# Performance work log

Measured on AMD Instinct MI355X. Metric: run time of the kernel, lower is better.

## Reference

```python
import jax, jax.numpy as jnp
import numpy as np

B, C, H, W = 2, 256, 360, 360
N1 = N2 = 1024


def setup_inputs() -> dict:
    key = jax.random.key(0)
    ks = jax.random.split(key, 12)
    s = 0.02
    feature = jax.random.normal(ks[0], (B, C, H, W), dtype=jnp.float32)
    # midx rows: [batch_idx, h, w]; frame 0 centers and frame 1 centers
    idx1 = jnp.stack([
        jnp.zeros((N1,), dtype=jnp.int32),
        jax.random.randint(ks[1], (N1,), 0, H, dtype=jnp.int32),
        jax.random.randint(ks[2], (N1,), 0, W, dtype=jnp.int32),
    ])
    idx2 = jnp.stack([
        jnp.ones((N2,), dtype=jnp.int32),
        jax.random.randint(ks[3], (N2,), 0, H, dtype=jnp.int32),
        jax.random.randint(ks[4], (N2,), 0, W, dtype=jnp.int32),
    ])
    w1 = jax.random.normal(ks[5], (256, 256), dtype=jnp.float32) * s
    b1 = jnp.zeros((256,), dtype=jnp.float32)
    w2 = jax.random.normal(ks[6], (256, 128), dtype=jnp.float32) * s
    b2 = jnp.zeros((128,), dtype=jnp.float32)
    w3 = jax.random.normal(ks[7], (128, 32), dtype=jnp.float32) * s
    b3 = jnp.zeros((32,), dtype=jnp.float32)
    w4 = jax.random.normal(ks[8], (32, 1), dtype=jnp.float32) * s
    b4 = jnp.zeros((1,), dtype=jnp.float32)
    return {"feature": feature, "idx1": idx1, "idx2": idx2,
            "w1": w1, "b1": b1, "w2": w2, "b2": b2,
            "w3": w3, "b3": b3, "w4": w4, "b4": b4}


def reference(feature, idx1, idx2, w1, b1, w2, b2, w3, b3, w4, b4):
    # feature: [B,C,H,W] -> [B,H,W,C] (torch .permute(0,2,3,1))
    feat = jnp.transpose(feature, (0, 2, 3, 1))

    def project(midx):
        # irregular gather of per-center features: [N, C]
        x = feat[midx[0], midx[1], midx[2]]
        h = jax.nn.relu(x @ w1 + b1)          # [N, 256]
        return jax.nn.relu(h @ w2 + b2)       # [N, 128]

    f1 = project(idx1)                        # [N1, D]
    f2 = project(idx2)                        # [N2, D]
    # laplacian_dists: broadcast outer difference [N1, N2, D]
    diff = f1[:, None, :] - f2[None, :, :]
    # out_layer = linear_last(D, 32, 1): Linear -> ReLU -> Linear
    h = jax.nn.relu(jnp.einsum('mnd,dk->mnk', diff, w3) + b3)
    out = jnp.einsum('mnk,ko->mno', h, w4) + b4
    return out[..., 0]                        # [N1, N2] similarity
```

## Files before the change

kernel.cpp:

```cpp
#include <hip/hip_runtime.h>

#define NPTS 1024
#define NC 256
#define NH 360
#define NW 360
#define NHW (NH * NW)
#define NCHW (NC * NHW)
#define PPB 8

__global__ __launch_bounds__(256) void gather_kernel(
    const float* __restrict__ feature,
    const int* __restrict__ idx1,
    const int* __restrict__ idx2,
    float* __restrict__ X)
{
    const int point = blockIdx.x;
    const int col = point & (NPTS - 1);
    const int* idx = (point < NPTS) ? idx1 : idx2;
    const int bb = idx[col];
    const int hh = idx[NPTS + col];
    const int ww = idx[2 * NPTS + col];
    const size_t base = (size_t)bb * NCHW + (size_t)hh * NW + ww;
    const int c = threadIdx.x;
    X[(size_t)point * NC + c] = feature[base + (size_t)c * NHW];
}

__global__ __launch_bounds__(512) void mlp_kernel(
    const float* __restrict__ X,
    const float* __restrict__ w1, const float* __restrict__ b1,
    const float* __restrict__ w2, const float* __restrict__ b2,
    const float* __restrict__ w3, const float* __restrict__ b3,
    float* __restrict__ pq)
{
    __shared__ float Xs[PPB * 256];
    __shared__ float H1s[PPB * 256];
    __shared__ float F2s[PPB * 128];

    const int tid = threadIdx.x;
    const int base = blockIdx.x * PPB;

    {
        const float* src = X + (size_t)base * 256;
        #pragma unroll
        for (int i = 0; i < PPB * 256; i += 512)
            Xs[i + tid] = src[i + tid];
    }
    __syncthreads();

    {
        const int j = tid & 255;
        const int half = tid >> 8;
        float acc[4] = {0.f, 0.f, 0.f, 0.f};
        #pragma unroll 4
        for (int c = 0; c < 256; ++c) {
            float wv = w1[c * 256 + j];
            #pragma unroll
            for (int q = 0; q < 4; ++q)
                acc[q] = fmaf(Xs[(half * 4 + q) * 256 + c], wv, acc[q]);
        }
        float bv = b1[j];
        #pragma unroll
        for (int q = 0; q < 4; ++q)
            H1s[(half * 4 + q) * 256 + j] = fmaxf(acc[q] + bv, 0.f);
    }
    __syncthreads();

    {
        const int j = tid & 127;
        const int quad = tid >> 7;
        float acc[2] = {0.f, 0.f};
        #pragma unroll 4
        for (int c = 0; c < 256; ++c) {
            float wv = w2[c * 128 + j];
            #pragma unroll
            for (int q = 0; q < 2; ++q)
                acc[q] = fmaf(H1s[(quad * 2 + q) * 256 + c], wv, acc[q]);
        }
        float bv = b2[j];
        #pragma unroll
        for (int q = 0; q < 2; ++q)
            F2s[(quad * 2 + q) * 128 + j] = fmaxf(acc[q] + bv, 0.f);
    }
    __syncthreads();

    if (tid < 256) {
        const int j = tid & 31;
        const int g = tid >> 5;
        float acc = 0.f;
        #pragma unroll 4
        for (int c = 0; c < 128; ++c)
            acc = fmaf(F2s[g * 128 + c], w3[c * 32 + j], acc);
        int point = base + g;
        float val = (point < NPTS) ? acc : (b3[j] - acc);
        pq[(size_t)point * 32 + j] = val;
    }
}

__global__ __launch_bounds__(256) void pair_kernel(
    const float* __restrict__ pq,
    const float* __restrict__ w4,
    const float* __restrict__ b4,
    float* __restrict__ out)
{
    __shared__ float P1s[8 * 32];
    __shared__ float w4s[32];

    const int tid = threadIdx.x;
    const int n = blockIdx.x * 256 + tid;
    const int m0 = blockIdx.y * 8;

    float q[32];
    const float* q2 = pq + (size_t)(NPTS + n) * 32;
    #pragma unroll
    for (int k = 0; k < 32; ++k) q[k] = q2[k];

    if (tid < 8 * 32) P1s[tid] = pq[(size_t)m0 * 32 + tid];
    if (tid < 32) w4s[tid] = w4[tid];
    __syncthreads();

    const float b4v = b4[0];
    #pragma unroll
    for (int mm = 0; mm < 8; ++mm) {
        float acc = b4v;
        #pragma unroll
        for (int k = 0; k < 32; ++k) {
            float t = P1s[mm * 32 + k] + q[k];
            acc = fmaf(w4s[k], fmaxf(t, 0.f), acc);
        }
        out[(size_t)(m0 + mm) * 1024 + n] = acc;
    }
}

extern "C" void kernel_launch(void* const* d_in, const int* in_sizes, int n_in,
                              void* d_out, int out_size, void* d_ws, size_t ws_size,
                              hipStream_t stream) {
    const float* feature = (const float*)d_in[0];
    const int*   idx1    = (const int*)d_in[1];
    const int*   idx2    = (const int*)d_in[2];
    const float* w1      = (const float*)d_in[3];
    const float* b1      = (const float*)d_in[4];
    const float* w2      = (const float*)d_in[5];
    const float* b2      = (const float*)d_in[6];
    const float* w3      = (const float*)d_in[7];
    const float* b3      = (const float*)d_in[8];
    const float* w4      = (const float*)d_in[9];
    const float* b4      = (const float*)d_in[10];
    float* out = (float*)d_out;

    float* X  = (float*)d_ws;
    float* pq = (float*)d_ws + 2048 * 256;

    gather_kernel<<<2048, 256, 0, stream>>>(feature, idx1, idx2, X);

    mlp_kernel<<<2048 / PPB, 512, 0, stream>>>(
        X, w1, b1, w2, b2, w3, b3, pq);

    pair_kernel<<<dim3(4, 128), 256, 0, stream>>>(pq, w4, b4, out);
}
```

Measured before the change: 402.3 us.

## Register-tile MLP layers with transposed padded shared memory and vectorized weight loads

New measurement: 380.1 us. -5.5%, faster.

```diff
diff --git a/kernel.cpp b/kernel.cpp
--- a/kernel.cpp
+++ b/kernel.cpp
@@ -7,6 +7,7 @@
 #define NHW (NH * NW)
 #define NCHW (NC * NHW)
 #define PPB 8
+#define PAD 12
 
 __global__ __launch_bounds__(256) void gather_kernel(
     const float* __restrict__ feature,
@@ -25,16 +26,16 @@
     X[(size_t)point * NC + c] = feature[base + (size_t)c * NHW];
 }
 
-__global__ __launch_bounds__(512) void mlp_kernel(
+__global__ __launch_bounds__(256) void mlp_kernel(
     const float* __restrict__ X,
     const float* __restrict__ w1, const float* __restrict__ b1,
     const float* __restrict__ w2, const float* __restrict__ b2,
     const float* __restrict__ w3, const float* __restrict__ b3,
     float* __restrict__ pq)
 {
-    __shared__ float Xs[PPB * 256];
-    __shared__ float H1s[PPB * 256];
-    __shared__ float F2s[PPB * 128];
+    __shared__ float Xs[256 * PAD];
+    __shared__ float H1s[256 * PAD];
+    __shared__ float F2s[128 * PAD];
 
     const int tid = threadIdx.x;
     const int base = blockIdx.x * PPB;
@@ -42,54 +43,74 @@
     {
         const float* src = X + (size_t)base * 256;
         #pragma unroll
-        for (int i = 0; i < PPB * 256; i += 512)
-            Xs[i + tid] = src[i + tid];
+        for (int p = 0; p < PPB; ++p)
+            Xs[tid * PAD + p] = src[p * 256 + tid];
+    }
+    __syncthreads();
+
+    const int jt = tid & 63;
+    const int pt = tid >> 6;
+    const int p0 = pt * 2;
+
+    {
+        const float4* w1v = (const float4*)w1;
+        float acc0[4] = {0.f, 0.f, 0.f, 0.f};
+        float acc1[4] = {0.f, 0.f, 0.f, 0.f};
+        #pragma unroll 8
+        for (int c = 0; c < 256; ++c) {
+            float4 wv = w1v[c * 64 + jt];
+            float a0 = Xs[c * PAD + p0];
+            float a1 = Xs[c * PAD + p0 + 1];
+            acc0[0] = fmaf(a0, wv.x, acc0[0]);
+            acc0[1] = fmaf(a0, wv.y, acc0[1]);
+            acc0[2] = fmaf(a0, wv.z, acc0[2]);
+            acc0[3] = fmaf(a0, wv.w, acc0[3]);
+            acc1[0] = fmaf(a1, wv.x, acc1[0]);
+            acc1[1] = fmaf(a1, wv.y, acc1[1]);
+            acc1[2] = fmaf(a1, wv.z, acc1[2]);
+            acc1[3] = fmaf(a1, wv.w, acc1[3]);
+        }
+        const int j0 = jt * 4;
+        #pragma unroll
+        for (int q = 0; q < 4; ++q) {
+            float bv = b1[j0 + q];
+            H1s[(j0 + q) * PAD + p0]     = fmaxf(acc0[q] + bv, 0.f);
+            H1s[(j0 + q) * PAD + p0 + 1] = fmaxf(acc1[q] + bv, 0.f);
+        }
     }
     __syncthreads();
 
     {
-        const int j = tid & 255;
-        const int half = tid >> 8;
-        float acc[4] = {0.f, 0.f, 0.f, 0.f};
-        #pragma unroll 4
+        const float2* w2v = (const float2*)w2;
+        float acc0[2] = {0.f, 0.f};
+        float acc1[2] = {0.f, 0.f};
+        #pragma unroll 8
         for (int c = 0; c < 256; ++c) {
-            float wv = w1[c * 256 + j];
-            #pragma unroll
-            for (int q = 0; q < 4; ++q)
-                acc[q] = fmaf(Xs[(half * 4 + q) * 256 + c], wv, acc[q]);
+            float2 wv = w2v[c * 64 + jt];
+            float a0 = H1s[c * PAD + p0];
+            float a1 = H1s[c * PAD + p0 + 1];
+            acc0[0] = fmaf(a0, wv.x, acc0[0]);
+            acc0[1] = fmaf(a0, wv.y, acc0[1]);
+            acc1[0] = fmaf(a1, wv.x, acc1[0]);
+            acc1[1] = fmaf(a1, wv.y, acc1[1]);
         }
-        float bv = b1[j];
+        const int j0 = jt * 2;
         #pragma unroll
-        for (int q = 0; q < 4; ++q)
-            H1s[(half * 4 + q) * 256 + j] = fmaxf(acc[q] + bv, 0.f);
+        for (int q = 0; q < 2; ++q) {
+            float bv = b2[j0 + q];
+            F2s[(j0 + q) * PAD + p0]     = fmaxf(acc0[q] + bv, 0.f);
+            F2s[(j0 + q) * PAD + p0 + 1] = fmaxf(acc1[q] + bv, 0.f);
+        }
     }
     __syncthreads();
 
     {
-        const int j = tid & 127;
-        const int quad = tid >> 7;
-        float acc[2] = {0.f, 0.f};
-        #pragma unroll 4
-        for (int c = 0; c < 256; ++c) {
-            float wv = w2[c * 128 + j];
-            #pragma unroll
-            for (int q = 0; q < 2; ++q)
-                acc[q] = fmaf(H1s[(quad * 2 + q) * 256 + c], wv, acc[q]);
-        }
-        float bv = b2[j];
-        #pragma unroll
-        for (int q = 0; q < 2; ++q)
-            F2s[(quad * 2 + q) * 128 + j] = fmaxf(acc[q] + bv, 0.f);
-    }
-    __syncthreads();
-
-    if (tid < 256) {
         const int j = tid & 31;
         const int g = tid >> 5;
         float acc = 0.f;
-        #pragma unroll 4
+        #pragma unroll 8
         for (int c = 0; c < 128; ++c)
-            acc = fmaf(F2s[g * 128 + c], w3[c * 32 + j], acc);
+            acc = fmaf(F2s[c * PAD + g], w3[c * 32 + j], acc);
         int point = base + g;
         float val = (point < NPTS) ? acc : (b3[j] - acc);
         pq[(size_t)point * 32 + j] = val;
@@ -152,7 +173,7 @@
 
     gather_kernel<<<2048, 256, 0, stream>>>(feature, idx1, idx2, X);
 
-    mlp_kernel<<<2048 / PPB, 512, 0, stream>>>(
+    mlp_kernel<<<2048 / PPB, 256, 0, stream>>>(
         X, w1, b1, w2, b2, w3, b3, pq);
 
     pair_kernel<<<dim3(4, 128), 256, 0, stream>>>(pq, w4, b4, out);
```

## Fuse gather into MLP kernel and remap threads to vectorized weight loads

Applied to the files above, without the earlier changes.

Result: faster. 376.6 us (-6.4%).

```diff
diff --git a/kernel.cpp b/kernel.cpp
--- a/kernel.cpp
+++ b/kernel.cpp
@@ -7,79 +7,80 @@
 #define NHW (NH * NW)
 #define NCHW (NC * NHW)
 #define PPB 8
+#define PAD 12
 
-__global__ __launch_bounds__(256) void gather_kernel(
+__global__ __launch_bounds__(512) void mlp_kernel(
     const float* __restrict__ feature,
     const int* __restrict__ idx1,
     const int* __restrict__ idx2,
-    float* __restrict__ X)
-{
-    const int point = blockIdx.x;
-    const int col = point & (NPTS - 1);
-    const int* idx = (point < NPTS) ? idx1 : idx2;
-    const int bb = idx[col];
-    const int hh = idx[NPTS + col];
-    const int ww = idx[2 * NPTS + col];
-    const size_t base = (size_t)bb * NCHW + (size_t)hh * NW + ww;
-    const int c = threadIdx.x;
-    X[(size_t)point * NC + c] = feature[base + (size_t)c * NHW];
-}
-
-__global__ __launch_bounds__(512) void mlp_kernel(
-    const float* __restrict__ X,
     const float* __restrict__ w1, const float* __restrict__ b1,
     const float* __restrict__ w2, const float* __restrict__ b2,
     const float* __restrict__ w3, const float* __restrict__ b3,
     float* __restrict__ pq)
 {
-    __shared__ float Xs[PPB * 256];
-    __shared__ float H1s[PPB * 256];
-    __shared__ float F2s[PPB * 128];
+    __shared__ float Xs[256 * PAD];
+    __shared__ float H1s[256 * PAD];
+    __shared__ float F2s[128 * PAD];
 
     const int tid = threadIdx.x;
     const int base = blockIdx.x * PPB;
 
     {
-        const float* src = X + (size_t)base * 256;
+        const int c = tid & 255;
+        const int pg = (tid >> 8) * 4;
+        float v[4];
         #pragma unroll
-        for (int i = 0; i < PPB * 256; i += 512)
-            Xs[i + tid] = src[i + tid];
+        for (int i = 0; i < 4; ++i) {
+            int point = base + pg + i;
+            int col = point & (NPTS - 1);
+            const int* idx = (point < NPTS) ? idx1 : idx2;
+            int bb = idx[col];
+            int hh = idx[NPTS + col];
+            int ww = idx[2 * NPTS + col];
+            v[i] = feature[(size_t)bb * NCHW + (size_t)c * NHW + hh * NW + ww];
+        }
+        #pragma unroll
+        for (int i = 0; i < 4; ++i)
+            Xs[c * PAD + pg + i] = v[i];
+    }
+    __syncthreads();
+
+    const int jt = tid & 63;
+    const int pt = tid >> 6;
+
+    {
+        const float4* w1v = (const float4*)w1;
+        float acc[4] = {0.f, 0.f, 0.f, 0.f};
+        #pragma unroll 8
+        for (int c = 0; c < 256; ++c) {
+            float4 wv = w1v[c * 64 + jt];
+            float a = Xs[c * PAD + pt];
+            acc[0] = fmaf(a, wv.x, acc[0]);
+            acc[1] = fmaf(a, wv.y, acc[1]);
+            acc[2] = fmaf(a, wv.z, acc[2]);
+            acc[3] = fmaf(a, wv.w, acc[3]);
+        }
+        const int j0 = jt * 4;
+        #pragma unroll
+        for (int q = 0; q < 4; ++q)
+            H1s[(j0 + q) * PAD + pt] = fmaxf(acc[q] + b1[j0 + q], 0.f);
     }
     __syncthreads();
 
     {
-        const int j = tid & 255;
-        const int half = tid >> 8;
-        float acc[4] = {0.f, 0.f, 0.f, 0.f};
-        #pragma unroll 4
+        const float2* w2v = (const float2*)w2;
+        float acc[2] = {0.f, 0.f};
+        #pragma unroll 8
         for (int c = 0; c < 256; ++c) {
-            float wv = w1[c * 256 + j];
-            #pragma unroll
-            for (int q = 0; q < 4; ++q)
-                acc[q] = fmaf(Xs[(half * 4 + q) * 256 + c], wv, acc[q]);
+            float2 wv = w2v[c * 64 + jt];
+            float a = H1s[c * PAD + pt];
+            acc[0] = fmaf(a, wv.x, acc[0]);
+            acc[1] = fmaf(a, wv.y, acc[1]);
         }
-        float bv = b1[j];
-        #pragma unroll
-        for (int q = 0; q < 4; ++q)
-            H1s[(half * 4 + q) * 256 + j] = fmaxf(acc[q] + bv, 0.f);
-    }
-    __syncthreads();
-
-    {
-        const int j = tid & 127;
-        const int quad = tid >> 7;
-        float acc[2] = {0.f, 0.f};
-        #pragma unroll 4
-        for (int c = 0; c < 256; ++c) {
-            float wv = w2[c * 128 + j];
-            #pragma unroll
-            for (int q = 0; q < 2; ++q)
-                acc[q] = fmaf(H1s[(quad * 2 + q) * 256 + c], wv, acc[q]);
-        }
-        float bv = b2[j];
+        const int j0 = jt * 2;
         #pragma unroll
         for (int q = 0; q < 2; ++q)
-            F2s[(quad * 2 + q) * 128 + j] = fmaxf(acc[q] + bv, 0.f);
+            F2s[(j0 + q) * PAD + pt] = fmaxf(acc[q] + b2[j0 + q], 0.f);
     }
     __syncthreads();
 
@@ -87,9 +88,9 @@
         const int j = tid & 31;
         const int g = tid >> 5;
         float acc = 0.f;
-        #pragma unroll 4
+        #pragma unroll 8
         for (int c = 0; c < 128; ++c)
-            acc = fmaf(F2s[g * 128 + c], w3[c * 32 + j], acc);
+            acc = fmaf(F2s[c * PAD + g], w3[c * 32 + j], acc);
         int point = base + g;
         float val = (point < NPTS) ? acc : (b3[j] - acc);
         pq[(size_t)point * 32 + j] = val;
@@ -147,13 +148,10 @@
     const float* b4      = (const float*)d_in[10];
     float* out = (float*)d_out;
 
-    float* X  = (float*)d_ws;
-    float* pq = (float*)d_ws + 2048 * 256;
-
-    gather_kernel<<<2048, 256, 0, stream>>>(feature, idx1, idx2, X);
+    float* pq = (float*)d_ws;
 
     mlp_kernel<<<2048 / PPB, 512, 0, stream>>>(
-        X, w1, b1, w2, b2, w3, b3, pq);
+        feature, idx1, idx2, w1, b1, w2, b2, w3, b3, pq);
 
     pair_kernel<<<dim3(4, 128), 256, 0, stream>>>(pq, w4, b4, out);
 }
```
